# Performance work log

Hardware: AMD Instinct MI355X
Metric: run time of the kernel (lower is better)

## Reference

```python
import jax, jax.numpy as jnp
import numpy as np

N = 100000      # nodes
E = 1600000     # edges (before self-loops)
IN = 64         # in_channels
HID = 16        # hidden_channels
HEADS = 4       # num_heads
G = 512         # number of graphs in batch
SLOPE = 0.2     # GATConv leaky_relu negative_slope


def setup_inputs() -> dict:
    key = jax.random.key(0)
    ks = jax.random.split(key, 12)
    s = 0.1
    x = jax.random.normal(ks[0], (N, IN), jnp.float32)
    edge_index = jax.random.randint(ks[1], (2, E), 0, N, dtype=jnp.int64)
    batch = jnp.sort(jax.random.randint(ks[2], (N,), 0, G, dtype=jnp.int64))
    W1 = jax.random.normal(ks[3], (IN, HEADS * HID), jnp.float32) * s
    a1_src = jax.random.normal(ks[4], (HEADS, HID), jnp.float32) * s
    a1_dst = jax.random.normal(ks[5], (HEADS, HID), jnp.float32) * s
    b1 = jnp.zeros((HEADS * HID,), jnp.float32)
    W2 = jax.random.normal(ks[6], (HEADS * HID, HID), jnp.float32) * s
    a2_src = jax.random.normal(ks[7], (1, HID), jnp.float32) * s
    a2_dst = jax.random.normal(ks[8], (1, HID), jnp.float32) * s
    b2 = jnp.zeros((HID,), jnp.float32)
    Wc = jax.random.normal(ks[9], (HID, 1), jnp.float32) * s
    bc = jnp.zeros((1,), jnp.float32)
    return dict(x=x, edge_index=edge_index, batch=batch, W1=W1, a1_src=a1_src,
                a1_dst=a1_dst, b1=b1, W2=W2, a2_src=a2_src, a2_dst=a2_dst,
                b2=b2, Wc=Wc, bc=bc)


def gat_layer(x, src, dst, W, a_s, a_d, bias, heads, out_ch, concat):
    # PyG GATConv: linear -> per-edge attention logits -> segment softmax over dst -> scatter aggregate
    n = x.shape[0]
    h = (x @ W).reshape(n, heads, out_ch)              # [N, H, C]
    al_s = jnp.sum(h * a_s, axis=-1)                   # [N, H]
    al_d = jnp.sum(h * a_d, axis=-1)                   # [N, H]
    e = al_s[src] + al_d[dst]                          # [E, H]
    e = jnp.where(e > 0, e, SLOPE * e)                 # leaky_relu
    m = jax.ops.segment_max(e, dst, num_segments=n)    # per-dst max (self-loops ensure non-empty)
    p = jnp.exp(e - m[dst])
    denom = jax.ops.segment_sum(p, dst, num_segments=n)
    alpha = p / (denom[dst] + 1e-16)                   # [E, H]
    out = jax.ops.segment_sum(h[src] * alpha[:, :, None], dst, num_segments=n)  # [N, H, C]
    out = out.reshape(n, heads * out_ch) if concat else out.mean(axis=1)
    return out + bias


def reference(x, edge_index, batch, W1, a1_src, a1_dst, b1, W2, a2_src, a2_dst, b2, Wc, bc):
    loops = jnp.arange(N, dtype=edge_index.dtype)      # GATConv add_self_loops=True
    src = jnp.concatenate([edge_index[0], loops])
    dst = jnp.concatenate([edge_index[1], loops])
    h = jax.nn.elu(gat_layer(x, src, dst, W1, a1_src, a1_dst, b1, HEADS, HID, True))
    # dropout inactive (eval mode)
    h = jax.nn.elu(gat_layer(h, src, dst, W2, a2_src, a2_dst, b2, 1, HID, False))
    counts = jax.ops.segment_sum(jnp.ones((N,), h.dtype), batch, num_segments=G)
    pooled = jax.ops.segment_sum(h, batch, num_segments=G) / jnp.maximum(counts, 1.0)[:, None]
    return pooled @ Wc + bc
```

## Files before the change

### kernel.cpp

```cpp
#include <hip/hip_runtime.h>
#include <hip/hip_fp16.h>
#include <hip/hip_fp8.h>

#define N_NODES 100000
#define N_EDGES 1600000
#define ET      (N_EDGES + N_NODES)
#define NG      512
#define SLOPE   0.2f

#define BKT_SHIFT 9
#define NB_B   ((N_NODES + 511) / 512)
#define BCAP   10240
#define CHUNK_A 8192
#define NBLK_A ((ET + CHUNK_A - 1) / CHUNK_A)
#define H1B4   ((N_NODES + 1023) / 1024)

typedef _Float16 half8_t __attribute__((ext_vector_type(8)));
typedef float    f32x4_t __attribute__((ext_vector_type(4)));
typedef float    f32x2_t __attribute__((ext_vector_type(2)));

__global__ __launch_bounds__(1024) void k_prepA(
    const float* __restrict__ x, const float* __restrict__ W1,
    const float* __restrict__ a1s, const float* __restrict__ a1d,
    const int* __restrict__ ei,
    int* __restrict__ gcnt, unsigned int* __restrict__ ebuf,
    __hip_fp8_e4m3* __restrict__ h1, float* __restrict__ al1s, float* __restrict__ al1d)
{
    __shared__ union U {
        struct { float Wl[64 * 64]; float asf[64]; float adf[64]; } p;
        struct { unsigned int stage[CHUNK_A]; unsigned char sbin[CHUNK_A];
                 int hist[NB_B]; int binst[NB_B]; int resv[NB_B]; int cur[NB_B];
                 int tmp[1024]; } a;
    } u;
    int tid = threadIdx.x;

    if (blockIdx.x < NBLK_A) {
        int base = blockIdx.x * CHUNK_A;
        int m = min(CHUNK_A, ET - base);
        for (int i = tid; i < NB_B; i += 1024) u.a.hist[i] = 0;
        __syncthreads();
        for (int i = tid; i < m; i += 1024) {
            int eid = base + i;
            int d = (eid < N_EDGES) ? ei[N_EDGES + eid] : (eid - N_EDGES);
            atomicAdd(&u.a.hist[d >> BKT_SHIFT], 1);
        }
        __syncthreads();
        int v = (tid < NB_B) ? u.a.hist[tid] : 0;
        u.a.tmp[tid] = v;
        __syncthreads();
        for (int off = 1; off < 1024; off <<= 1) {
            int t = (tid >= off) ? u.a.tmp[tid - off] : 0;
            __syncthreads();
            u.a.tmp[tid] += t;
            __syncthreads();
        }
        if (tid < NB_B) {
            int e = u.a.tmp[tid] - v;
            u.a.binst[tid] = e;
            u.a.cur[tid] = e;
            u.a.resv[tid] = v ? atomicAdd(&gcnt[tid], v) : 0;
        }
        __syncthreads();
        for (int i = tid; i < m; i += 1024) {
            int eid = base + i;
            int s, d;
            if (eid < N_EDGES) { s = ei[eid]; d = ei[N_EDGES + eid]; }
            else               { s = eid - N_EDGES; d = s; }
            int b = d >> BKT_SHIFT;
            int pos = atomicAdd(&u.a.cur[b], 1);
            u.a.stage[pos] = ((unsigned int)(d & 511) << 17) | (unsigned int)s;
            u.a.sbin[pos] = (unsigned char)b;
        }
        __syncthreads();
        for (int i = tid; i < m; i += 1024) {
            int b = u.a.sbin[i];
            ebuf[b * BCAP + u.a.resv[b] + (i - u.a.binst[b])] = u.a.stage[i];
        }
        return;
    }

    for (int i = tid; i < 64 * 64; i += 1024) u.p.Wl[i] = W1[i];
    if (tid < 64) { u.p.asf[tid] = a1s[tid]; u.p.adf[tid] = a1d[tid]; }
    __syncthreads();

    int wv = tid >> 6, lane = tid & 63;
    int m = lane & 15, q = lane >> 4;

    half8_t bf[4][2];
#pragma unroll
    for (int t = 0; t < 4; ++t)
#pragma unroll
        for (int s = 0; s < 2; ++s) {
            half8_t b;
#pragma unroll
            for (int j = 0; j < 8; ++j)
                b[j] = (_Float16)u.p.Wl[(s * 32 + q * 8 + j) * 64 + t * 16 + m];
            bf[t][s] = b;
        }

    int nodebase = (blockIdx.x - NBLK_A) * 1024 + wv * 64;
    for (int it = 0; it < 4; ++it) {
        int node0 = nodebase + it * 16;
        int node = node0 + m;
        half8_t av0 = {}, av1 = {};
        if (node < N_NODES) {
            const float4* xr = (const float4*)(x + (long long)node * 64);
            float4 p0 = xr[q * 2], p1 = xr[q * 2 + 1];
            float4 p2 = xr[q * 2 + 8], p3 = xr[q * 2 + 9];
            av0[0] = (_Float16)p0.x; av0[1] = (_Float16)p0.y;
            av0[2] = (_Float16)p0.z; av0[3] = (_Float16)p0.w;
            av0[4] = (_Float16)p1.x; av0[5] = (_Float16)p1.y;
            av0[6] = (_Float16)p1.z; av0[7] = (_Float16)p1.w;
            av1[0] = (_Float16)p2.x; av1[1] = (_Float16)p2.y;
            av1[2] = (_Float16)p2.z; av1[3] = (_Float16)p2.w;
            av1[4] = (_Float16)p3.x; av1[5] = (_Float16)p3.y;
            av1[6] = (_Float16)p3.z; av1[7] = (_Float16)p3.w;
        }
        f32x4_t acc[4] = {{0,0,0,0},{0,0,0,0},{0,0,0,0},{0,0,0,0}};
#pragma unroll
        for (int t = 0; t < 4; ++t) {
            acc[t] = __builtin_amdgcn_mfma_f32_16x16x32_f16(av0, bf[t][0], acc[t], 0, 0, 0);
            acc[t] = __builtin_amdgcn_mfma_f32_16x16x32_f16(av1, bf[t][1], acc[t], 0, 0, 0);
        }
#pragma unroll
        for (int r = 0; r < 4; ++r) {
            int nr = node0 + q * 4 + r;
            bool ok = nr < N_NODES;
#pragma unroll
            for (int t = 0; t < 4; ++t) {
                float v = acc[t][r];
                if (ok) h1[(long long)nr * 64 + t * 16 + m] = __hip_fp8_e4m3(v);
                float ps = v * u.p.asf[t * 16 + m];
                float pd = v * u.p.adf[t * 16 + m];
                ps += __shfl_xor(ps, 1); ps += __shfl_xor(ps, 2);
                ps += __shfl_xor(ps, 4); ps += __shfl_xor(ps, 8);
                pd += __shfl_xor(pd, 1); pd += __shfl_xor(pd, 2);
                pd += __shfl_xor(pd, 4); pd += __shfl_xor(pd, 8);
                if (ok && m == t) { al1s[nr * 4 + t] = ps; al1d[nr * 4 + t] = pd; }
            }
        }
    }
}

__global__ __launch_bounds__(1024) void k_passB(
    const unsigned int* __restrict__ ebuf, const int* __restrict__ gcnt,
    int* __restrict__ csr, int* __restrict__ offs, int* __restrict__ deg)
{
    __shared__ int ldeg[512];
    __shared__ int lofs[512];
    __shared__ int lcur[512];
    int tid = threadIdx.x;
    int b = blockIdx.x;
    int nb0 = b << BKT_SHIFT;
    int nn = min(512, N_NODES - nb0);
    int gbase = b * BCAP, cnt = gcnt[b];
    if (tid < 512) ldeg[tid] = 0;
    __syncthreads();
    for (int i = tid; i < cnt; i += 1024)
        atomicAdd(&ldeg[ebuf[gbase + i] >> 17], 1);
    __syncthreads();
    int v = 0;
    if (tid < 512) { v = ldeg[tid]; lofs[tid] = v; }
    __syncthreads();
    for (int off = 1; off < 512; off <<= 1) {
        int t = (tid >= off && tid < 512) ? lofs[tid - off] : 0;
        __syncthreads();
        if (tid < 512) lofs[tid] += t;
        __syncthreads();
    }
    if (tid < 512) {
        int e = lofs[tid] - v;
        lcur[tid] = e;
        if (tid < nn) { offs[nb0 + tid] = gbase + e; deg[nb0 + tid] = v; }
    }
    __syncthreads();
    for (int i = tid; i < cnt; i += 1024) {
        unsigned int ev = ebuf[gbase + i];
        int dl = ev >> 17, s = (int)(ev & 0x1FFFF);
        int p = atomicAdd(&lcur[dl], 1);
        csr[gbase + p] = s;
    }
}

__global__ __launch_bounds__(256) void k_agg1(
    const int* __restrict__ offs, const int* __restrict__ deg, const int* __restrict__ csr,
    const __hip_fp8_e4m3* __restrict__ h1, const float* __restrict__ al1s, const float* __restrict__ al1d,
    const float* __restrict__ b1, const float* __restrict__ W2,
    const float* __restrict__ a2s, const float* __restrict__ a2d,
    __half* __restrict__ h2, float* __restrict__ al2s, float* __restrict__ al2d)
{
    __shared__ int   sarr[4][64];
    __shared__ float warr[4][4 * 72];
    __shared__ __align__(16) float h1b[4][64];
    __shared__ __align__(16) float W2t[16][66];
    __shared__ float a2sl[16], a2dl[16];
    int tid = threadIdx.x;
    for (int i = tid; i < 64 * 16; i += 256) W2t[i & 15][i >> 4] = W2[i];
    if (tid < 16) { a2sl[tid] = a2s[tid]; a2dl[tid] = a2d[tid]; }
    __syncthreads();

    int wv = tid >> 6, lane = tid & 63;
    int eslot = lane >> 4;
    int cq = lane & 15;
    int hh = cq >> 2;
    int cq4 = cq * 4;
    int node = blockIdx.x * 4 + wv;
    int st = offs[node], dg = deg[node];
    const float4 ald4 = *(const float4*)(al1d + node * 4);
    float b1l = b1[lane];
    const char* __restrict__ h1c = (const char*)h1;

    f32x2_t a01 = {0.f, 0.f}, a23 = {0.f, 0.f};
    float den = 0.f;
    for (int base = 0; base < dg; base += 64) {
        int m = min(64, dg - base);
        int s = 0;
        float w0 = 0.f, w1 = 0.f, w2 = 0.f, w3 = 0.f;
        if (lane < m) {
            s = csr[st + base + lane];
            const float4 as4 = *(const float4*)(al1s + s * 4);
            float e0 = as4.x + ald4.x; e0 = e0 > 0.f ? e0 : SLOPE * e0;
            float e1 = as4.y + ald4.y; e1 = e1 > 0.f ? e1 : SLOPE * e1;
            float e2 = as4.z + ald4.z; e2 = e2 > 0.f ? e2 : SLOPE * e2;
            float e3 = as4.w + ald4.w; e3 = e3 > 0.f ? e3 : SLOPE * e3;
            w0 = __expf(e0); w1 = __expf(e1); w2 = __expf(e2); w3 = __expf(e3);
        }
        sarr[wv][lane] = s << 6;
        warr[wv][0 * 72 + lane] = w0;
        warr[wv][1 * 72 + lane] = w1;
        warr[wv][2 * 72 + lane] = w2;
        warr[wv][3 * 72 + lane] = w3;
        int m4 = (m + 3) & ~3;
#pragma unroll 4
        for (int j0 = 0; j0 < m4; j0 += 4) {
            int j = j0 + eslot;
            int off = sarr[wv][j] + cq4;
            float wgt = warr[wv][hh * 72 + j];
            unsigned int pk = *(const unsigned int*)(h1c + off);
            f32x2_t wg2 = {wgt, wgt};
            a01 = __builtin_elementwise_fma(wg2, __builtin_amdgcn_cvt_pk_f32_fp8((int)pk, false), a01);
            a23 = __builtin_elementwise_fma(wg2, __builtin_amdgcn_cvt_pk_f32_fp8((int)pk, true),  a23);
            den += wgt;
        }
    }
    a01.x += __shfl_xor(a01.x, 16); a01.x += __shfl_xor(a01.x, 32);
    a01.y += __shfl_xor(a01.y, 16); a01.y += __shfl_xor(a01.y, 32);
    a23.x += __shfl_xor(a23.x, 16); a23.x += __shfl_xor(a23.x, 32);
    a23.y += __shfl_xor(a23.y, 16); a23.y += __shfl_xor(a23.y, 32);
    den   += __shfl_xor(den, 16);   den   += __shfl_xor(den, 32);
    if (lane < 16)
        *(float4*)&h1b[wv][cq4] = make_float4(a01.x, a01.y, a23.x, a23.y);
    float denc = __shfl(den, (lane >> 4) << 2);
    __builtin_amdgcn_wave_barrier();
    float v = h1b[wv][lane] / (denc + 1e-16f) + b1l;
    v = v > 0.f ? v : __expf(v) - 1.f;
    h1b[wv][lane] = v;
    __builtin_amdgcn_wave_barrier();

    int c2 = lane & 15, slot = lane >> 4;
    f32x2_t acc2 = {0.f, 0.f};
#pragma unroll
    for (int i = 0; i < 8; ++i) {
        int k = slot * 16 + i * 2;
        f32x2_t hv  = *(const f32x2_t*)&h1b[wv][k];
        f32x2_t wv2 = *(const f32x2_t*)&W2t[c2][k];
        acc2 = __builtin_elementwise_fma(hv, wv2, acc2);
    }
    float h2val = acc2.x + acc2.y;
    h2val += __shfl_xor(h2val, 16);
    h2val += __shfl_xor(h2val, 32);
    float ps2 = h2val * a2sl[c2];
    float pd2 = h2val * a2dl[c2];
    ps2 += __shfl_xor(ps2, 1); ps2 += __shfl_xor(ps2, 2);
    ps2 += __shfl_xor(ps2, 4); ps2 += __shfl_xor(ps2, 8);
    pd2 += __shfl_xor(pd2, 1); pd2 += __shfl_xor(pd2, 2);
    pd2 += __shfl_xor(pd2, 4); pd2 += __shfl_xor(pd2, 8);
    if (lane < 16) h2[node * 16 + c2] = __float2half_rn(h2val);
    if (lane == 0) { al2s[node] = ps2; al2d[node] = pd2; }
}

__global__ __launch_bounds__(256) void k_agg2(
    const int* __restrict__ offs, const int* __restrict__ deg, const int* __restrict__ csr,
    const __half* __restrict__ h2, const float* __restrict__ al2s, const float* __restrict__ al2d,
    const float* __restrict__ b2, const int* __restrict__ batch, float* __restrict__ pooled)
{
    __shared__ int    sarr[4][64];
    __shared__ float  warr[4][64];
    __shared__ float2 pl[4][8];
    __shared__ int    gl[4];
    int tid = threadIdx.x;
    int wv = tid >> 6, lane = tid & 63;
    int ec = lane >> 3, cc = lane & 7;
    int node = blockIdx.x * 4 + wv;
    int st = offs[node], dg = deg[node];
    float ald = al2d[node];
    const __half2* __restrict__ h2v = (const __half2*)h2;

    float a0 = 0.f, a1 = 0.f, den = 0.f;
    for (int base = 0; base < dg; base += 64) {
        int m = min(64, dg - base);
        int s = 0; float wl = 0.f;
        if (lane < m) {
            s = csr[st + base + lane];
            float e = al2s[s] + ald;
            e = e > 0.f ? e : SLOPE * e;
            wl = __expf(e);
        }
        sarr[wv][lane] = s;
        warr[wv][lane] = wl;
        float t = wl;
#pragma unroll
        for (int x = 1; x < 64; x <<= 1) t += __shfl_xor(t, x);
        den += t;
        int m8 = (m + 7) & ~7;
#pragma unroll 2
        for (int j0 = 0; j0 < m8; j0 += 8) {
            int j = j0 + ec;
            int s2i = sarr[wv][j];
            float wgt = warr[wv][j];
            __half2 hv = h2v[s2i * 8 + cc];
            a0 = fmaf(__low2float(hv), wgt, a0);
            a1 = fmaf(__high2float(hv), wgt, a1);
        }
    }
    a0 += __shfl_xor(a0, 8);  a1 += __shfl_xor(a1, 8);
    a0 += __shfl_xor(a0, 16); a1 += __shfl_xor(a1, 16);
    a0 += __shfl_xor(a0, 32); a1 += __shfl_xor(a1, 32);
    if (lane < 8) {
        float inv = 1.f / (den + 1e-16f);
        float v0 = a0 * inv + b2[2 * cc];
        float v1 = a1 * inv + b2[2 * cc + 1];
        v0 = v0 > 0.f ? v0 : __expf(v0) - 1.f;
        v1 = v1 > 0.f ? v1 : __expf(v1) - 1.f;
        pl[wv][cc] = make_float2(v0, v1);
    }
    if (lane == 0) gl[wv] = batch[node];
    __syncthreads();
    if (wv == 0 && lane < 8) {
        int g0 = gl[0], g3 = gl[3];
        if (g0 == g3) {
            float2 s0 = pl[0][lane], s1 = pl[1][lane], s2 = pl[2][lane], s3 = pl[3][lane];
            atomicAdd(&pooled[g0 * 16 + 2 * lane],     s0.x + s1.x + s2.x + s3.x);
            atomicAdd(&pooled[g0 * 16 + 2 * lane + 1], s0.y + s1.y + s2.y + s3.y);
        } else {
#pragma unroll
            for (int nd = 0; nd < 4; ++nd) {
                float2 s = pl[nd][lane];
                atomicAdd(&pooled[gl[nd] * 16 + 2 * lane],     s.x);
                atomicAdd(&pooled[gl[nd] * 16 + 2 * lane + 1], s.y);
            }
        }
    }
}

__global__ __launch_bounds__(256) void k_cls(
    const float* __restrict__ pooled, const int* __restrict__ batch,
    const float* __restrict__ Wc, const float* __restrict__ bc, float* __restrict__ out)
{
    int g = blockIdx.x * 256 + threadIdx.x;
    if (g >= NG) return;
    int lo = 0, hi = N_NODES;
    while (lo < hi) { int mid = (lo + hi) >> 1; if (batch[mid] < g) lo = mid + 1; else hi = mid; }
    int s = lo;
    lo = 0; hi = N_NODES;
    while (lo < hi) { int mid = (lo + hi) >> 1; if (batch[mid] < g + 1) lo = mid + 1; else hi = mid; }
    float cnt = fmaxf((float)(lo - s), 1.0f);
    float acc = 0.f;
#pragma unroll
    for (int c = 0; c < 16; ++c) acc += pooled[g * 16 + c] * Wc[c];
    out[g] = acc / cnt + bc[0];
}

extern "C" void kernel_launch(void* const* d_in, const int* in_sizes, int n_in,
                              void* d_out, int out_size, void* d_ws, size_t ws_size,
                              hipStream_t stream)
{
    const float* x    = (const float*)d_in[0];
    const int*   ei   = (const int*)d_in[1];
    const int*   batc = (const int*)d_in[2];
    const float* W1   = (const float*)d_in[3];
    const float* a1s  = (const float*)d_in[4];
    const float* a1d  = (const float*)d_in[5];
    const float* b1   = (const float*)d_in[6];
    const float* W2   = (const float*)d_in[7];
    const float* a2s  = (const float*)d_in[8];
    const float* a2d  = (const float*)d_in[9];
    const float* b2   = (const float*)d_in[10];
    const float* Wc   = (const float*)d_in[11];
    const float* bc   = (const float*)d_in[12];
    float* out = (float*)d_out;

    char* ws = (char*)d_ws;
    size_t off = 0;
    auto carveB = [&](size_t bytes) {
        void* p = ws + off;
        off += ((bytes + 15) & ~(size_t)15);
        return p;
    };
    auto carve = [&](size_t elems) { return carveB(elems * 4); };
    int*   gcnt   = (int*)  carve(NB_B);
    float* pooled = (float*)carve((size_t)NG * 16);
    size_t zero_bytes = off;
    unsigned int* ebuf = (unsigned int*)carve((size_t)NB_B * BCAP);
    int*   csr    = (int*)  carve((size_t)NB_B * BCAP);
    int*   offs   = (int*)  carve(N_NODES);
    int*   deg    = (int*)  carve(N_NODES);
    __hip_fp8_e4m3* h1 = (__hip_fp8_e4m3*)carveB((size_t)N_NODES * 64);
    float* al1s   = (float*)carve((size_t)N_NODES * 4);
    float* al1d   = (float*)carve((size_t)N_NODES * 4);
    __half* h2    = (__half*)carveB((size_t)N_NODES * 16 * 2);
    float* al2s   = (float*)carve(N_NODES);
    float* al2d   = (float*)carve(N_NODES);

    hipMemsetAsync(d_ws, 0, zero_bytes, stream);

    k_prepA<<<NBLK_A + H1B4, 1024, 0, stream>>>(x, W1, a1s, a1d, ei, gcnt, ebuf, h1, al1s, al1d);
    k_passB<<<NB_B, 1024, 0, stream>>>(ebuf, gcnt, csr, offs, deg);
    k_agg1 <<<N_NODES / 4, 256, 0, stream>>>(offs, deg, csr, h1, al1s, al1d, b1,
                                             W2, a2s, a2d, h2, al2s, al2d);
    k_agg2 <<<N_NODES / 4, 256, 0, stream>>>(offs, deg, csr, h2, al2s, al2d, b2, batc, pooled);
    k_cls  <<<NG / 256, 256, 0, stream>>>(pooled, batc, Wc, bc, out);
}
```

Measured before the change: 280.3 us.

## Split layer-2 projection out of agg1 into MFMA-based k_mid kernel

Moves the per-node 64x16 W2 projection and layer-2 attention logits out of the aggregation kernel into a separate kernel that uses f16 MFMA on 16-node tiles. The aggregation kernel now writes the ELU-activated layer-1 output as fp16 to global memory, dropping its W2 shared-memory load, a block barrier and the scalar dot-product work. The fp8 unpacking also moves from packed to scalar conversions, and agg2 accumulates the softmax denominator per lane instead of doing a full-wave reduction each chunk. In exchange it adds an extra launch plus a 12.8MB fp16 intermediate write and read, and rounds layer-1 activations to fp16 before the projection.

```diff
diff --git a/kernel.cpp b/kernel.cpp
--- a/kernel.cpp
+++ b/kernel.cpp
@@ -17,7 +17,6 @@
 
 typedef _Float16 half8_t __attribute__((ext_vector_type(8)));
 typedef float    f32x4_t __attribute__((ext_vector_type(4)));
-typedef float    f32x2_t __attribute__((ext_vector_type(2)));
 
 __global__ __launch_bounds__(1024) void k_prepA(
     const float* __restrict__ x, const float* __restrict__ W1,
@@ -185,24 +184,16 @@
 __global__ __launch_bounds__(256) void k_agg1(
     const int* __restrict__ offs, const int* __restrict__ deg, const int* __restrict__ csr,
     const __hip_fp8_e4m3* __restrict__ h1, const float* __restrict__ al1s, const float* __restrict__ al1d,
-    const float* __restrict__ b1, const float* __restrict__ W2,
-    const float* __restrict__ a2s, const float* __restrict__ a2d,
-    __half* __restrict__ h2, float* __restrict__ al2s, float* __restrict__ al2d)
+    const float* __restrict__ b1, __half* __restrict__ h1bg)
 {
     __shared__ int   sarr[4][64];
     __shared__ float warr[4][4 * 72];
     __shared__ __align__(16) float h1b[4][64];
-    __shared__ __align__(16) float W2t[16][66];
-    __shared__ float a2sl[16], a2dl[16];
     int tid = threadIdx.x;
-    for (int i = tid; i < 64 * 16; i += 256) W2t[i & 15][i >> 4] = W2[i];
-    if (tid < 16) { a2sl[tid] = a2s[tid]; a2dl[tid] = a2d[tid]; }
-    __syncthreads();
-
     int wv = tid >> 6, lane = tid & 63;
     int eslot = lane >> 4;
     int cq = lane & 15;
-    int hh = cq >> 2;
+    int h = cq >> 2;
     int cq4 = cq * 4;
     int node = blockIdx.x * 4 + wv;
     int st = offs[node], dg = deg[node];
@@ -210,8 +201,7 @@
     float b1l = b1[lane];
     const char* __restrict__ h1c = (const char*)h1;
 
-    f32x2_t a01 = {0.f, 0.f}, a23 = {0.f, 0.f};
-    float den = 0.f;
+    float a0 = 0.f, a1 = 0.f, a2 = 0.f, a3 = 0.f, den = 0.f;
     for (int base = 0; base < dg; base += 64) {
         int m = min(64, dg - base);
         int s = 0;
@@ -235,48 +225,72 @@
         for (int j0 = 0; j0 < m4; j0 += 4) {
             int j = j0 + eslot;
             int off = sarr[wv][j] + cq4;
-            float wgt = warr[wv][hh * 72 + j];
+            float wgt = warr[wv][h * 72 + j];
             unsigned int pk = *(const unsigned int*)(h1c + off);
-            f32x2_t wg2 = {wgt, wgt};
-            a01 = __builtin_elementwise_fma(wg2, __builtin_amdgcn_cvt_pk_f32_fp8((int)pk, false), a01);
-            a23 = __builtin_elementwise_fma(wg2, __builtin_amdgcn_cvt_pk_f32_fp8((int)pk, true),  a23);
+            a0 = fmaf(wgt, __builtin_amdgcn_cvt_f32_fp8(pk, 0), a0);
+            a1 = fmaf(wgt, __builtin_amdgcn_cvt_f32_fp8(pk, 1), a1);
+            a2 = fmaf(wgt, __builtin_amdgcn_cvt_f32_fp8(pk, 2), a2);
+            a3 = fmaf(wgt, __builtin_amdgcn_cvt_f32_fp8(pk, 3), a3);
             den += wgt;
         }
     }
-    a01.x += __shfl_xor(a01.x, 16); a01.x += __shfl_xor(a01.x, 32);
-    a01.y += __shfl_xor(a01.y, 16); a01.y += __shfl_xor(a01.y, 32);
-    a23.x += __shfl_xor(a23.x, 16); a23.x += __shfl_xor(a23.x, 32);
-    a23.y += __shfl_xor(a23.y, 16); a23.y += __shfl_xor(a23.y, 32);
-    den   += __shfl_xor(den, 16);   den   += __shfl_xor(den, 32);
+    a0 += __shfl_xor(a0, 16); a0 += __shfl_xor(a0, 32);
+    a1 += __shfl_xor(a1, 16); a1 += __shfl_xor(a1, 32);
+    a2 += __shfl_xor(a2, 16); a2 += __shfl_xor(a2, 32);
+    a3 += __shfl_xor(a3, 16); a3 += __shfl_xor(a3, 32);
+    den += __shfl_xor(den, 16); den += __shfl_xor(den, 32);
     if (lane < 16)
-        *(float4*)&h1b[wv][cq4] = make_float4(a01.x, a01.y, a23.x, a23.y);
+        *(float4*)&h1b[wv][cq4] = make_float4(a0, a1, a2, a3);
     float denc = __shfl(den, (lane >> 4) << 2);
-    __builtin_amdgcn_wave_barrier();
     float v = h1b[wv][lane] / (denc + 1e-16f) + b1l;
     v = v > 0.f ? v : __expf(v) - 1.f;
-    h1b[wv][lane] = v;
-    __builtin_amdgcn_wave_barrier();
-
-    int c2 = lane & 15, slot = lane >> 4;
-    f32x2_t acc2 = {0.f, 0.f};
-#pragma unroll
-    for (int i = 0; i < 8; ++i) {
-        int k = slot * 16 + i * 2;
-        f32x2_t hv  = *(const f32x2_t*)&h1b[wv][k];
-        f32x2_t wv2 = *(const f32x2_t*)&W2t[c2][k];
-        acc2 = __builtin_elementwise_fma(hv, wv2, acc2);
-    }
-    float h2val = acc2.x + acc2.y;
-    h2val += __shfl_xor(h2val, 16);
-    h2val += __shfl_xor(h2val, 32);
-    float ps2 = h2val * a2sl[c2];
-    float pd2 = h2val * a2dl[c2];
-    ps2 += __shfl_xor(ps2, 1); ps2 += __shfl_xor(ps2, 2);
-    ps2 += __shfl_xor(ps2, 4); ps2 += __shfl_xor(ps2, 8);
-    pd2 += __shfl_xor(pd2, 1); pd2 += __shfl_xor(pd2, 2);
-    pd2 += __shfl_xor(pd2, 4); pd2 += __shfl_xor(pd2, 8);
-    if (lane < 16) h2[node * 16 + c2] = __float2half_rn(h2val);
-    if (lane == 0) { al2s[node] = ps2; al2d[node] = pd2; }
+    h1bg[(long long)node * 64 + lane] = __float2half_rn(v);
+}
+
+__global__ __launch_bounds__(256) void k_mid(
+    const __half* __restrict__ h1bg, const float* __restrict__ W2,
+    const float* __restrict__ a2s, const float* __restrict__ a2d,
+    __half* __restrict__ h2, float* __restrict__ al2s, float* __restrict__ al2d)
+{
+    __shared__ float W2l[64 * 16];
+    int tid = threadIdx.x;
+    for (int i = tid; i < 64 * 16; i += 256) W2l[i] = W2[i];
+    __syncthreads();
+    int wv = tid >> 6, lane = tid & 63;
+    int m = lane & 15, q = lane >> 4;
+    half8_t bf[2];
+#pragma unroll
+    for (int s = 0; s < 2; ++s) {
+        half8_t b;
+#pragma unroll
+        for (int j = 0; j < 8; ++j)
+            b[j] = (_Float16)W2l[(s * 32 + q * 8 + j) * 16 + m];
+        bf[s] = b;
+    }
+    int node0 = blockIdx.x * 64 + wv * 16;
+    half8_t av0 = {}, av1 = {};
+    if (node0 + m < N_NODES) {
+        const __half* ar = h1bg + (long long)(node0 + m) * 64;
+        av0 = *(const half8_t*)(ar + q * 8);
+        av1 = *(const half8_t*)(ar + 32 + q * 8);
+    }
+    f32x4_t acc = {0, 0, 0, 0};
+    acc = __builtin_amdgcn_mfma_f32_16x16x32_f16(av0, bf[0], acc, 0, 0, 0);
+    acc = __builtin_amdgcn_mfma_f32_16x16x32_f16(av1, bf[1], acc, 0, 0, 0);
+    float a2sm = a2s[m], a2dm = a2d[m];
+#pragma unroll
+    for (int r = 0; r < 4; ++r) {
+        int nr = node0 + q * 4 + r;
+        bool ok = nr < N_NODES;
+        float v = acc[r];
+        if (ok) h2[nr * 16 + m] = __float2half_rn(v);
+        float ps = v * a2sm, pd = v * a2dm;
+        ps += __shfl_xor(ps, 1); ps += __shfl_xor(ps, 2);
+        ps += __shfl_xor(ps, 4); ps += __shfl_xor(ps, 8);
+        pd += __shfl_xor(pd, 1); pd += __shfl_xor(pd, 2);
+        pd += __shfl_xor(pd, 4); pd += __shfl_xor(pd, 8);
+        if (ok && m == 0) { al2s[nr] = ps; al2d[nr] = pd; }
+    }
 }
 
 __global__ __launch_bounds__(256) void k_agg2(
@@ -308,10 +322,6 @@
         }
         sarr[wv][lane] = s;
         warr[wv][lane] = wl;
-        float t = wl;
-#pragma unroll
-        for (int x = 1; x < 64; x <<= 1) t += __shfl_xor(t, x);
-        den += t;
         int m8 = (m + 7) & ~7;
 #pragma unroll 2
         for (int j0 = 0; j0 < m8; j0 += 8) {
@@ -321,11 +331,12 @@
             __half2 hv = h2v[s2i * 8 + cc];
             a0 = fmaf(__low2float(hv), wgt, a0);
             a1 = fmaf(__high2float(hv), wgt, a1);
-        }
-    }
-    a0 += __shfl_xor(a0, 8);  a1 += __shfl_xor(a1, 8);
-    a0 += __shfl_xor(a0, 16); a1 += __shfl_xor(a1, 16);
-    a0 += __shfl_xor(a0, 32); a1 += __shfl_xor(a1, 32);
+            den += wgt;
+        }
+    }
+    a0 += __shfl_xor(a0, 8);  a1 += __shfl_xor(a1, 8);  den += __shfl_xor(den, 8);
+    a0 += __shfl_xor(a0, 16); a1 += __shfl_xor(a1, 16); den += __shfl_xor(den, 16);
+    a0 += __shfl_xor(a0, 32); a1 += __shfl_xor(a1, 32); den += __shfl_xor(den, 32);
     if (lane < 8) {
         float inv = 1.f / (den + 1e-16f);
         float v0 = a0 * inv + b2[2 * cc];
@@ -408,6 +419,7 @@
     __hip_fp8_e4m3* h1 = (__hip_fp8_e4m3*)carveB((size_t)N_NODES * 64);
     float* al1s   = (float*)carve((size_t)N_NODES * 4);
     float* al1d   = (float*)carve((size_t)N_NODES * 4);
+    __half* h1bg  = (__half*)carveB((size_t)N_NODES * 64 * 2);
     __half* h2    = (__half*)carveB((size_t)N_NODES * 16 * 2);
     float* al2s   = (float*)carve(N_NODES);
     float* al2d   = (float*)carve(N_NODES);
@@ -416,8 +428,8 @@
 
     k_prepA<<<NBLK_A + H1B4, 1024, 0, stream>>>(x, W1, a1s, a1d, ei, gcnt, ebuf, h1, al1s, al1d);
     k_passB<<<NB_B, 1024, 0, stream>>>(ebuf, gcnt, csr, offs, deg);
-    k_agg1 <<<N_NODES / 4, 256, 0, stream>>>(offs, deg, csr, h1, al1s, al1d, b1,
-                                             W2, a2s, a2d, h2, al2s, al2d);
+    k_agg1 <<<N_NODES / 4, 256, 0, stream>>>(offs, deg, csr, h1, al1s, al1d, b1, h1bg);
+    k_mid  <<<(N_NODES + 63) / 64, 256, 0, stream>>>(h1bg, W2, a2s, a2d, h2, al2s, al2d);
     k_agg2 <<<N_NODES / 4, 256, 0, stream>>>(offs, deg, csr, h2, al2s, al2d, b2, batc, pooled);
     k_cls  <<<NG / 256, 256, 0, stream>>>(pooled, batc, Wc, bc, out);
 }
```

Result: faster. 269.1 us (-4.0%).
